# Performance work log

Hardware: AMD Instinct MI355X
Metric: run time of the kernel (lower is better)

Reference implementation:

```python
import jax, jax.numpy as jnp
import numpy as np

B, S, H = 2, 2048, 1024
NH, HD = 16, 64
WINDOW = 512
NEG = -10000.0


def setup_inputs() -> dict:
    key = jax.random.key(0)
    ks = jax.random.split(key, 8)
    sc = 0.02
    return {
        "hidden_states": jax.random.normal(ks[0], (B, S, H), dtype=jnp.float32),
        "attention_mask": jnp.zeros((B, 1, 1, S), dtype=jnp.float32),
        "Wq": jax.random.normal(ks[1], (H, H), dtype=jnp.float32) * sc,
        "bq": jnp.zeros((H,), dtype=jnp.float32),
        "Wk": jax.random.normal(ks[2], (H, H), dtype=jnp.float32) * sc,
        "bk": jnp.zeros((H,), dtype=jnp.float32),
        "Wv": jax.random.normal(ks[3], (H, H), dtype=jnp.float32) * sc,
        "bv": jnp.zeros((H,), dtype=jnp.float32),
    }


def _heads(x):
    # [b, t, (h d)] -> [b, h, t, d]
    b, t, _ = x.shape
    return x.reshape(b, t, NH, HD).transpose(0, 2, 1, 3)


def reference(hidden_states, attention_mask, Wq, bq, Wk, bk, Wv, bv):
    q = _heads(hidden_states @ Wq.T + bq)
    k = _heads(hidden_states @ Wk.T + bk)
    v = _heads(hidden_states @ Wv.T + bv)

    # Faithful mask construction (note: window mask is triu(diag=-WINDOW),
    # penalizing the recent window, exactly as in the source).
    i = jnp.arange(S)[:, None]
    j = jnp.arange(S)[None, :]
    causal_mask = jnp.where(j > i, NEG, 0.0).astype(jnp.float32)          # triu, diag=1
    window_mask = jnp.where(j >= i - WINDOW, NEG, 0.0).astype(jnp.float32)  # triu, diag=-512
    mask = causal_mask + window_mask + attention_mask  # [b,1,S,S]

    scale = 1.0 / jnp.sqrt(jnp.asarray(HD, dtype=q.dtype))
    scores = jnp.einsum("bhtd,bhsd->bhts", q, k) * scale + mask  # [b,h,S,S]
    probs = jax.nn.softmax(scores, axis=-1)
    out = jnp.einsum("bhts,bhsd->bhtd", probs, v)  # [b,h,S,d]
    # [b,h,t,d] -> [b,t,(h d)]
    return out.transpose(0, 2, 1, 3).reshape(B, S, H)
```

## Files before the change

### kernel.cpp

```cpp
#include <hip/hip_runtime.h>

typedef float f32x2 __attribute__((ext_vector_type(2)));
typedef float f32x4 __attribute__((ext_vector_type(4)));
typedef float f32x16 __attribute__((ext_vector_type(16)));
typedef _Float16 half8 __attribute__((ext_vector_type(8)));
typedef _Float16 half4 __attribute__((ext_vector_type(4)));
typedef unsigned int u32;
typedef u32 u32x4 __attribute__((ext_vector_type(4)));

#define S_LEN 2048
#define NHEAD 16
#define HDIM 64
#define BATCH 2
#define WINDOW 512
#define M2_FIX 5.770780163555852f
#define LOG2E 1.4426950408889634f

#define GLDS16(gp, lp) __builtin_amdgcn_global_load_lds( \
    (const __attribute__((address_space(1))) void*)(gp), \
    (__attribute__((address_space(3))) void*)(lp), 16, 0, 0)


__global__ __launch_bounds__(256) void convert_kernel(
    const float4* __restrict__ hs, const float4* __restrict__ wq,
    const float4* __restrict__ wk, const float4* __restrict__ wv,
    _Float16* __restrict__ hsb, _Float16* __restrict__ wb) {
  int i = blockIdx.x * 256 + threadIdx.x;
  float4 v;
  _Float16* dst;
  if (i < 1048576) {
    v = hs[i];
    dst = hsb + (size_t)i * 4;
  } else {
    int j = i - 1048576;
    if (j < 262144) v = wq[j];
    else if (j < 524288) v = wk[j - 262144];
    else v = wv[j - 524288];
    dst = wb + (size_t)j * 4;
  }
  half4 o;
  o[0] = (_Float16)v.x; o[1] = (_Float16)v.y;
  o[2] = (_Float16)v.z; o[3] = (_Float16)v.w;
  *(half4*)dst = o;
}

__global__ __launch_bounds__(256) void qkv_gemm(
    const _Float16* __restrict__ A, const _Float16* __restrict__ W,
    const float* __restrict__ bq, const float* __restrict__ bk,
    const float* __restrict__ bv,
    _Float16* __restrict__ Qf, _Float16* __restrict__ Kf, _Float16* __restrict__ Vf) {
  __shared__ _Float16 sbuf[2][16384];
  const int tid = threadIdx.x;
  const int wv = tid >> 6;
  const int lane = tid & 63;
  const int g = lane >> 4;
  const int c = lane & 15;
  const int b = blockIdx.x;
  const int xcd = b & 7;
  const int s = b >> 3;
  const int sub = s / 48;
  const int rem = s - sub * 48;
  const int m0 = (((xcd >> 1) << 3) + rem / 6) * 128;
  const int n0 = ((xcd & 1) * 12 + sub * 6 + rem % 6) * 128;
  const int wm = (wv & 1) * 64;
  const int wn = (wv >> 1) * 64;

  const int srow8 = lane >> 3;
  const int sslot = lane & 7;
  const int lsl = sslot ^ srow8;
  const int rA = wv * 32 + srow8;
  const _Float16* aS = A + (size_t)(m0 + rA) * 1024 + lsl * 8;
  const _Float16* bS = W + (size_t)(n0 + rA) * 1024 + lsl * 8;

  const int rcolA0 = wv * 32 * 64;

  f32x4 acc[4][4];
#pragma unroll
  for (int i = 0; i < 4; ++i)
#pragma unroll
    for (int j = 0; j < 4; ++j) acc[i][j] = (f32x4){0.f, 0.f, 0.f, 0.f};

  auto STAGE = [&](int bf_, int k0) __attribute__((always_inline)) {
    char* aD = (char*)&sbuf[bf_][rcolA0];
    char* bD = (char*)&sbuf[bf_][8192 + rcolA0];
#pragma unroll
    for (int grp = 0; grp < 4; ++grp) {
      GLDS16(aS + grp * 8192 + k0, aD + grp * 1024);
      GLDS16(bS + grp * 8192 + k0, bD + grp * 1024);
    }
  };

  STAGE(0, 0);
  __syncthreads();
  int cur = 0;

  for (int t = 0; t < 16; ++t) {
    if (t < 15) STAGE(cur ^ 1, (t + 1) * 64);
    const _Float16* Asb = &sbuf[cur][0];
    const _Float16* Bsb = &sbuf[cur][8192];
    half8 af[4][2];
#pragma unroll
    for (int mf = 0; mf < 4; ++mf) {
      const int row = wm + mf * 16 + c;
#pragma unroll
      for (int ch = 0; ch < 2; ++ch)
        af[mf][ch] = *(const half8*)&Asb[row * 64 + ((ch * 4 + g) ^ (c & 7)) * 8];
    }
#pragma unroll
    for (int nf = 0; nf < 4; ++nf) {
      const int row = wn + nf * 16 + c;
      half8 bf0 = *(const half8*)&Bsb[row * 64 + ((g) ^ (c & 7)) * 8];
      half8 bf1 = *(const half8*)&Bsb[row * 64 + ((4 + g) ^ (c & 7)) * 8];
#pragma unroll
      for (int mf = 0; mf < 4; ++mf) {
        acc[mf][nf] = __builtin_amdgcn_mfma_f32_16x16x32_f16(af[mf][0], bf0, acc[mf][nf], 0, 0, 0);
        acc[mf][nf] = __builtin_amdgcn_mfma_f32_16x16x32_f16(af[mf][1], bf1, acc[mf][nf], 0, 0, 0);
      }
    }
    __syncthreads();
    cur ^= 1;
  }

  const int kind = n0 >> 10;
  const int nb = (n0 + wn) & 1023;
  const int head = nb >> 6;
  const float* bias = kind == 0 ? bq : (kind == 1 ? bk : bv);
  _Float16* dst = kind == 0 ? Qf : (kind == 1 ? Kf : Vf);
  _Float16* ob = &sbuf[0][wv * 4096];

  if (kind < 2) {
    const float scl = kind == 0 ? (0.125f * LOG2E) : 1.0f;
#pragma unroll
    for (int nf = 0; nf < 4; ++nf) {
      const int d = nf * 16 + c;
      const float bsv = bias[nb + d];
      const int base = nf * 512 + ((c >> 3) & 1) * 256 + (c & 7);
#pragma unroll
      for (int mf = 0; mf < 4; ++mf) {
#pragma unroll
        for (int r = 0; r < 4; ++r) {
          ob[(mf >> 1) * 2048 + base + (mf & 1) * 128 + g * 32 + r * 8] =
              (_Float16)((acc[mf][nf][r] + bsv) * scl);
        }
      }
    }
  } else {
#pragma unroll
    for (int nf = 0; nf < 4; ++nf) {
      const int d = nf * 16 + c;
      const float bsv = bias[nb + d];
#pragma unroll
      for (int mf = 0; mf < 4; ++mf) {
        half4 v4;
#pragma unroll
        for (int r = 0; r < 4; ++r) v4[r] = (_Float16)(acc[mf][nf][r] + bsv);
        *(half4*)&ob[(mf >> 1) * 2048 + ((nf >> 1) * 2 + (mf & 1)) * 512 +
                     ((g >> 1) * 32 + (nf & 1) * 16 + c) * 8 + (g & 1) * 4] = v4;
      }
    }
  }

  const int bI = (m0 + wm) >> 11;
  const size_t gbase = (size_t)(bI * NHEAD + head) * 131072 +
                       (size_t)(((m0 + wm) & 2047) >> 5) * 2048;
#pragma unroll
  for (int i = 0; i < 8; ++i) {
    half8 v = *(const half8*)&ob[i * 512 + lane * 8];
    *(half8*)&dst[gbase + i * 512 + lane * 8] = v;
  }
}

__global__ __launch_bounds__(256) void attn_kernel(
    const _Float16* __restrict__ Qf, const _Float16* __restrict__ Kf,
    const _Float16* __restrict__ Vf, const float* __restrict__ amask,
    float* __restrict__ out) {
  __shared__ _Float16 obuf[4][32][72];
  __shared__ float lbuf[4][32];
  const int tid = threadIdx.x;
  const int w = tid >> 6;
  const int lane = tid & 63;
  const int q31 = lane & 31;
  const int h = lane >> 5;
  const int bid = blockIdx.x;
  const int xcd = bid & 7;
  const int bh = xcd * 4 + ((bid >> 3) & 3);
  const int idx = 63 - (bid >> 5);
  const int i0 = idx * 32;
  const int bI = bh >> 4;
  const int head = bh & 15;

  const _Float16* Qh = Qf + (size_t)bh * 131072;
  const _Float16* Kh = Kf + (size_t)bh * 131072;
  const _Float16* Vh = Vf + (size_t)bh * 131072;
  const float* am = amask + (size_t)bI * S_LEN;

  const int q = i0 + q31;
  const int hiq = (q <= WINDOW) ? q : (q - WINDOW - 1);
  const int last = i0 + 31;
  const int himax = (last <= WINDOW) ? last
                    : ((i0 <= WINDOW) ? WINDOW : (last - WINDOW - 1));
  const int hiq_min = (last <= WINDOW) ? i0
                      : ((i0 > WINDOW) ? (i0 - WINDOW - 1) : 0);
  const int ntiles = (himax >> 5) + 1;
  const int nfull = (hiq_min + 1) >> 5;
  const int lim = hiq - 4 * h;

  half8 qf[4];
#pragma unroll
  for (int ch = 0; ch < 4; ++ch)
    qf[ch] = *(const half8*)&Qh[(size_t)idx * 2048 + ch * 512 + lane * 8];

  f32x16 zero16, m2init;
#pragma unroll
  for (int r = 0; r < 16; ++r) { zero16[r] = 0.f; m2init[r] = -M2_FIX; }
  f32x16 oacc0 = zero16, oacc1 = zero16;
  f32x2 lp[4];
#pragma unroll
  for (int r = 0; r < 4; ++r) lp[r] = (f32x2){0.f, 0.f};

  auto computeTile = [&](half8 k0, half8 k1, half8 k2, half8 k3,
                         half8 vf0, half8 vf1, half8 vf2, half8 vf3, int t)
      __attribute__((always_inline)) {
    const int j0 = t * 32;
    f32x4 amv[4];
#pragma unroll
    for (int s4 = 0; s4 < 4; ++s4)
      amv[s4] = *(const f32x4*)&am[j0 + 8 * s4 + 4 * h];

    __builtin_amdgcn_s_setprio(1);
    f32x16 st = __builtin_amdgcn_mfma_f32_32x32x16_f16(k0, qf[0], m2init, 0, 0, 0);
    st = __builtin_amdgcn_mfma_f32_32x32x16_f16(k1, qf[1], st, 0, 0, 0);
    st = __builtin_amdgcn_mfma_f32_32x32x16_f16(k2, qf[2], st, 0, 0, 0);
    st = __builtin_amdgcn_mfma_f32_32x32x16_f16(k3, qf[3], st, 0, 0, 0);
    __builtin_amdgcn_s_setprio(0);

    float p[16];
#pragma unroll
    for (int r = 0; r < 16; ++r)
      p[r] = __builtin_fmaf(amv[r >> 2][r & 3], LOG2E, st[r]);
    if (t >= nfull) {
      const int lm = lim - j0;
#pragma unroll
      for (int r = 0; r < 16; ++r) {
        const int off = (r & 3) + 8 * (r >> 2);
        p[r] = (off <= lm) ? p[r] : -3e38f;
      }
    }
#pragma unroll
    for (int r = 0; r < 16; ++r) p[r] = __builtin_amdgcn_exp2f(p[r]);
#pragma unroll
    for (int j = 0; j < 4; ++j) {
      lp[j] += (f32x2){p[2 * j], p[2 * j + 1]};
      lp[j] += (f32x2){p[8 + 2 * j], p[9 + 2 * j]};
    }

    u32 pk[8];
#pragma unroll
    for (int r = 0; r < 8; ++r) {
      auto c2 = __builtin_amdgcn_cvt_pkrtz(p[2 * r], p[2 * r + 1]);
      pk[r] = __builtin_bit_cast(u32, c2);
    }
    u32 a0 = pk[0], b0 = pk[2];
    u32 a1 = pk[1], b1 = pk[3];
    u32 a2 = pk[4], b2 = pk[6];
    u32 a3 = pk[5], b3 = pk[7];
    asm("v_permlane32_swap_b32 %0, %1" : "+v"(a0), "+v"(b0));
    asm("v_permlane32_swap_b32 %0, %1" : "+v"(a1), "+v"(b1));
    asm("v_permlane32_swap_b32 %0, %1" : "+v"(a2), "+v"(b2));
    asm("v_permlane32_swap_b32 %0, %1" : "+v"(a3), "+v"(b3));
    const half8 pf0 = __builtin_bit_cast(half8, (u32x4){a0, a1, b0, b1});
    const half8 pf1 = __builtin_bit_cast(half8, (u32x4){a2, a3, b2, b3});

    __builtin_amdgcn_s_setprio(1);
    oacc0 = __builtin_amdgcn_mfma_f32_32x32x16_f16(vf0, pf0, oacc0, 0, 0, 0);
    oacc0 = __builtin_amdgcn_mfma_f32_32x32x16_f16(vf1, pf1, oacc0, 0, 0, 0);
    oacc1 = __builtin_amdgcn_mfma_f32_32x32x16_f16(vf2, pf0, oacc1, 0, 0, 0);
    oacc1 = __builtin_amdgcn_mfma_f32_32x32x16_f16(vf3, pf1, oacc1, 0, 0, 0);
    __builtin_amdgcn_s_setprio(0);
  };

#define LOADKV(k0, k1, k2, k3, v0, v1, v2, v3, tt)                       \
  {                                                                      \
    const _Float16* kt = Kh + (size_t)(tt) * 2048 + lane * 8;            \
    const _Float16* vt = Vh + (size_t)(tt) * 2048 + lane * 8;            \
    k0 = *(const half8*)&kt[0];                                          \
    k1 = *(const half8*)&kt[512];                                        \
    k2 = *(const half8*)&kt[1024];                                       \
    k3 = *(const half8*)&kt[1536];                                       \
    v0 = *(const half8*)&vt[0];                                          \
    v1 = *(const half8*)&vt[512];                                        \
    v2 = *(const half8*)&vt[1024];                                       \
    v3 = *(const half8*)&vt[1536];                                       \
  }

  int t = w;
  if (t < ntiles) {
    half8 k0, k1, k2, k3, v0, v1, v2, v3;
    LOADKV(k0, k1, k2, k3, v0, v1, v2, v3, t);
    int tn = t + 4;
    while (tn < ntiles) {
      half8 n0, n1, n2, n3, u0, u1, u2, u3;
      LOADKV(n0, n1, n2, n3, u0, u1, u2, u3, tn);
      computeTile(k0, k1, k2, k3, v0, v1, v2, v3, t);
      k0 = n0; k1 = n1; k2 = n2; k3 = n3;
      v0 = u0; v1 = u1; v2 = u2; v3 = u3;
      t = tn;
      tn += 4;
    }
    computeTile(k0, k1, k2, k3, v0, v1, v2, v3, t);
  }

  f32x2 s2 = (lp[0] + lp[1]) + (lp[2] + lp[3]);
  float lw = s2[0] + s2[1];
  lw += __shfl_xor(lw, 32);
  if (h == 0) lbuf[w][q31] = lw;
#pragma unroll
  for (int j = 0; j < 4; ++j) {
    half4 h0, h1;
#pragma unroll
    for (int e = 0; e < 4; ++e) {
      h0[e] = (_Float16)oacc0[4 * j + e];
      h1[e] = (_Float16)oacc1[4 * j + e];
    }
    *(half4*)&obuf[w][q31][4 * h + 8 * j]      = h0;
    *(half4*)&obuf[w][q31][32 + 4 * h + 8 * j] = h1;
  }
  __syncthreads();

  const int mq = tid >> 3;
  const int md = (tid & 7) * 8;
  const float lt = (lbuf[0][mq] + lbuf[1][mq]) + (lbuf[2][mq] + lbuf[3][mq]);
  float s[8];
  half8 p0 = *(const half8*)&obuf[0][mq][md];
#pragma unroll
  for (int e = 0; e < 8; ++e) s[e] = (float)p0[e];
#pragma unroll
  for (int w4 = 1; w4 < 4; ++w4) {
    half8 pw = *(const half8*)&obuf[w4][mq][md];
#pragma unroll
    for (int e = 0; e < 8; ++e) s[e] += (float)pw[e];
  }
  const float inv = 1.0f / lt;
  float4 s0, s1;
  s0.x = s[0] * inv; s0.y = s[1] * inv; s0.z = s[2] * inv; s0.w = s[3] * inv;
  s1.x = s[4] * inv; s1.y = s[5] * inv; s1.z = s[6] * inv; s1.w = s[7] * inv;
  float* op = out + ((size_t)(bI * S_LEN + i0 + mq)) * 1024 + head * 64 + md;
  *(float4*)op = s0;
  *(float4*)(op + 4) = s1;
}

extern "C" void kernel_launch(void* const* d_in, const int* in_sizes, int n_in,
                              void* d_out, int out_size, void* d_ws, size_t ws_size,
                              hipStream_t stream) {
  const float* hs = (const float*)d_in[0];
  const float* am = (const float*)d_in[1];
  const float* Wq = (const float*)d_in[2];
  const float* bq = (const float*)d_in[3];
  const float* Wk = (const float*)d_in[4];
  const float* bk = (const float*)d_in[5];
  const float* Wv = (const float*)d_in[6];
  const float* bv = (const float*)d_in[7];
  float* out = (float*)d_out;

  char* ws = (char*)d_ws;
  _Float16* hsb = (_Float16*)(ws);
  _Float16* wb  = (_Float16*)(ws + 8388608);
  _Float16* Qf  = (_Float16*)(ws + 14680064);
  _Float16* Kf  = (_Float16*)(ws + 23068672);
  _Float16* Vf  = (_Float16*)(ws + 31457280);

  convert_kernel<<<7168, 256, 0, stream>>>(
      (const float4*)hs, (const float4*)Wq, (const float4*)Wk, (const float4*)Wv, hsb, wb);
  qkv_gemm<<<768, 256, 0, stream>>>(hsb, wb, bq, bk, bv, Qf, Kf, Vf);
  attn_kernel<<<2048, 256, 0, stream>>>(Qf, Kf, Vf, am, out);
}
```

Baseline: 77.17 us.

## Enlarge QKV GEMM tiles, prefetch mask with K/V, remap attention blocks

The QKV projection GEMM now uses 256x128 output tiles with 512 threads (8 waves) and a larger LDS double buffer, halving the grid to 384 blocks. This gives more reuse of the staged weight tiles per block. The attention kernel now loads the additive mask vector in the same software-pipelined prefetch as the next K/V tile, instead of loading it inside the compute step. It also maps blocks to (batch, head) with a plain modulo rather than an XCD-aware grouping, which may change L2 locality of K/V across chiplets.

```diff
diff --git a/kernel.cpp b/kernel.cpp
--- a/kernel.cpp
+++ b/kernel.cpp
@@ -44,12 +44,12 @@
   *(half4*)dst = o;
 }
 
-__global__ __launch_bounds__(256) void qkv_gemm(
+__global__ __launch_bounds__(512) void qkv_gemm(
     const _Float16* __restrict__ A, const _Float16* __restrict__ W,
     const float* __restrict__ bq, const float* __restrict__ bk,
     const float* __restrict__ bv,
     _Float16* __restrict__ Qf, _Float16* __restrict__ Kf, _Float16* __restrict__ Vf) {
-  __shared__ _Float16 sbuf[2][16384];
+  __shared__ _Float16 sbuf[2][24576];
   const int tid = threadIdx.x;
   const int wv = tid >> 6;
   const int lane = tid & 63;
@@ -58,21 +58,20 @@
   const int b = blockIdx.x;
   const int xcd = b & 7;
   const int s = b >> 3;
-  const int sub = s / 48;
-  const int rem = s - sub * 48;
-  const int m0 = (((xcd >> 1) << 3) + rem / 6) * 128;
-  const int n0 = ((xcd & 1) * 12 + sub * 6 + rem % 6) * 128;
-  const int wm = (wv & 1) * 64;
-  const int wn = (wv >> 1) * 64;
+  const int m0 = ((xcd >> 2) * 8 + (s & 7)) * 256;
+  const int n0 = ((xcd & 3) * 6 + (s >> 3)) * 128;
+  const int wm = (wv & 3) * 64;
+  const int wn = (wv >> 2) * 64;
+  const _Float16* Asb0;
+  const _Float16* Bsb0;
 
   const int srow8 = lane >> 3;
   const int sslot = lane & 7;
   const int lsl = sslot ^ srow8;
-  const int rA = wv * 32 + srow8;
-  const _Float16* aS = A + (size_t)(m0 + rA) * 1024 + lsl * 8;
-  const _Float16* bS = W + (size_t)(n0 + rA) * 1024 + lsl * 8;
-
-  const int rcolA0 = wv * 32 * 64;
+  const _Float16* aS = A + (size_t)(m0 + wv * 32 + srow8) * 1024 + lsl * 8;
+  const _Float16* bS = W + (size_t)(n0 + wv * 16 + srow8) * 1024 + lsl * 8;
+  const int aBase = wv * 2048;
+  const int bBase = 16384 + wv * 1024;
 
   f32x4 acc[4][4];
 #pragma unroll
@@ -81,13 +80,14 @@
     for (int j = 0; j < 4; ++j) acc[i][j] = (f32x4){0.f, 0.f, 0.f, 0.f};
 
   auto STAGE = [&](int bf_, int k0) __attribute__((always_inline)) {
-    char* aD = (char*)&sbuf[bf_][rcolA0];
-    char* bD = (char*)&sbuf[bf_][8192 + rcolA0];
-#pragma unroll
-    for (int grp = 0; grp < 4; ++grp) {
+    char* aD = (char*)&sbuf[bf_][aBase];
+    char* bD = (char*)&sbuf[bf_][bBase];
+#pragma unroll
+    for (int grp = 0; grp < 4; ++grp)
       GLDS16(aS + grp * 8192 + k0, aD + grp * 1024);
+#pragma unroll
+    for (int grp = 0; grp < 2; ++grp)
       GLDS16(bS + grp * 8192 + k0, bD + grp * 1024);
-    }
   };
 
   STAGE(0, 0);
@@ -97,7 +97,7 @@
   for (int t = 0; t < 16; ++t) {
     if (t < 15) STAGE(cur ^ 1, (t + 1) * 64);
     const _Float16* Asb = &sbuf[cur][0];
-    const _Float16* Bsb = &sbuf[cur][8192];
+    const _Float16* Bsb = &sbuf[cur][16384];
     half8 af[4][2];
 #pragma unroll
     for (int mf = 0; mf < 4; ++mf) {
@@ -126,7 +126,7 @@
   const int head = nb >> 6;
   const float* bias = kind == 0 ? bq : (kind == 1 ? bk : bv);
   _Float16* dst = kind == 0 ? Qf : (kind == 1 ? Kf : Vf);
-  _Float16* ob = &sbuf[0][wv * 4096];
+  _Float16* ob = &sbuf[0][0] + wv * 4096;
 
   if (kind < 2) {
     const float scl = kind == 0 ? (0.125f * LOG2E) : 1.0f;
@@ -182,8 +182,7 @@
   const int q31 = lane & 31;
   const int h = lane >> 5;
   const int bid = blockIdx.x;
-  const int xcd = bid & 7;
-  const int bh = xcd * 4 + ((bid >> 3) & 3);
+  const int bh = bid & 31;
   const int idx = 63 - (bid >> 5);
   const int i0 = idx * 32;
   const int bI = bh >> 4;
@@ -219,13 +218,11 @@
   for (int r = 0; r < 4; ++r) lp[r] = (f32x2){0.f, 0.f};
 
   auto computeTile = [&](half8 k0, half8 k1, half8 k2, half8 k3,
-                         half8 vf0, half8 vf1, half8 vf2, half8 vf3, int t)
+                         half8 vf0, half8 vf1, half8 vf2, half8 vf3,
+                         f32x4 am0, f32x4 am1, f32x4 am2, f32x4 am3, int t)
       __attribute__((always_inline)) {
     const int j0 = t * 32;
-    f32x4 amv[4];
-#pragma unroll
-    for (int s4 = 0; s4 < 4; ++s4)
-      amv[s4] = *(const f32x4*)&am[j0 + 8 * s4 + 4 * h];
+    f32x4 amv[4] = {am0, am1, am2, am3};
 
     __builtin_amdgcn_s_setprio(1);
     f32x16 st = __builtin_amdgcn_mfma_f32_32x32x16_f16(k0, qf[0], m2init, 0, 0, 0);
@@ -279,10 +276,11 @@
     __builtin_amdgcn_s_setprio(0);
   };
 
-#define LOADKV(k0, k1, k2, k3, v0, v1, v2, v3, tt)                       \
+#define LOADALL(k0, k1, k2, k3, v0, v1, v2, v3, a0_, a1_, a2_, a3_, tt)  \
   {                                                                      \
     const _Float16* kt = Kh + (size_t)(tt) * 2048 + lane * 8;            \
     const _Float16* vt = Vh + (size_t)(tt) * 2048 + lane * 8;            \
+    const float* at = am + (tt) * 32 + 4 * h;                            \
     k0 = *(const half8*)&kt[0];                                          \
     k1 = *(const half8*)&kt[512];                                        \
     k2 = *(const half8*)&kt[1024];                                       \
@@ -291,23 +289,30 @@
     v1 = *(const half8*)&vt[512];                                        \
     v2 = *(const half8*)&vt[1024];                                       \
     v3 = *(const half8*)&vt[1536];                                       \
+    a0_ = *(const f32x4*)&at[0];                                         \
+    a1_ = *(const f32x4*)&at[8];                                         \
+    a2_ = *(const f32x4*)&at[16];                                        \
+    a3_ = *(const f32x4*)&at[24];                                        \
   }
 
   int t = w;
   if (t < ntiles) {
     half8 k0, k1, k2, k3, v0, v1, v2, v3;
-    LOADKV(k0, k1, k2, k3, v0, v1, v2, v3, t);
+    f32x4 a0, a1, a2, a3;
+    LOADALL(k0, k1, k2, k3, v0, v1, v2, v3, a0, a1, a2, a3, t);
     int tn = t + 4;
     while (tn < ntiles) {
       half8 n0, n1, n2, n3, u0, u1, u2, u3;
-      LOADKV(n0, n1, n2, n3, u0, u1, u2, u3, tn);
-      computeTile(k0, k1, k2, k3, v0, v1, v2, v3, t);
+      f32x4 e0, e1, e2, e3;
+      LOADALL(n0, n1, n2, n3, u0, u1, u2, u3, e0, e1, e2, e3, tn);
+      computeTile(k0, k1, k2, k3, v0, v1, v2, v3, a0, a1, a2, a3, t);
       k0 = n0; k1 = n1; k2 = n2; k3 = n3;
       v0 = u0; v1 = u1; v2 = u2; v3 = u3;
+      a0 = e0; a1 = e1; a2 = e2; a3 = e3;
       t = tn;
       tn += 4;
     }
-    computeTile(k0, k1, k2, k3, v0, v1, v2, v3, t);
+    computeTile(k0, k1, k2, k3, v0, v1, v2, v3, a0, a1, a2, a3, t);
   }
 
   f32x2 s2 = (lp[0] + lp[1]) + (lp[2] + lp[3]);
@@ -371,6 +376,6 @@
 
   convert_kernel<<<7168, 256, 0, stream>>>(
       (const float4*)hs, (const float4*)Wq, (const float4*)Wk, (const float4*)Wv, hsb, wb);
-  qkv_gemm<<<768, 256, 0, stream>>>(hsb, wb, bq, bk, bv, Qf, Kf, Vf);
+  qkv_gemm<<<384, 512, 0, stream>>>(hsb, wb, bq, bk, bv, Qf, Kf, Vf);
   attn_kernel<<<2048, 256, 0, stream>>>(Qf, Kf, Vf, am, out);
 }
```

Result: no change. 78.05 us (+1.1%).
